# Kernel optimization log

Measured on AMD Instinct MI355X. Metric: run time of the kernel, lower is better.

Reference implementation:

```python
import jax, jax.numpy as jnp
import numpy as np
from jax import lax

T_D = 0.7          # condensation radius
T_B = 0.2          # min beta to seed a condensate
FEATURE_LENGTH = 9 # columns of raw features before the prediction block
N_FEAT = 17        # n_ccoords = N_FEAT - 14 = 3
N_EVENTS = 16
POINTS_PER_EVENT = 65536


def setup_inputs() -> dict:
    key = jax.random.key(0)
    N = N_EVENTS * POINTS_PER_EVENT
    # uniform [0,1): betas in [0,1), ccoords in the unit cube -> realistic clustering
    x = jax.random.uniform(key, (N, N_FEAT), dtype=jnp.float32)
    row_splits = (jnp.arange(N_EVENTS + 1) * POINTS_PER_EVENT).astype(jnp.int32)
    return {"x": x, "row_splits": row_splits}


def _build_condensates(ccoords, betas, radius, min_beta):
    """Greedy NMS-like condensation, vectorized over events.
    ccoords: [E, P, C] float; betas: [E, P] float.
    Returns asso [E,P] int32 (index of assigned condensate, -1 = noise) and
    iscond [E,P] bool (condensation point flags).
    """
    E, P, _ = ccoords.shape
    r2 = radius * radius

    def masked_beta(asso):
        return jnp.where(asso < 0, betas, -1.0)

    def cond_fn(state):
        asso, _ = state
        return jnp.any(jnp.max(masked_beta(asso), axis=1) >= min_beta)

    def body_fn(state):
        asso, iscond = state
        mb = masked_beta(asso)                     # [E,P]
        ref = jnp.argmax(mb, axis=1)               # [E] highest-beta unassigned point
        valid = jnp.take_along_axis(mb, ref[:, None], axis=1)[:, 0] >= min_beta  # [E]
        refc = jnp.take_along_axis(ccoords, ref[:, None, None], axis=1)          # [E,1,C]
        distsq = jnp.sum((ccoords - refc) ** 2, axis=-1)                          # [E,P]
        assign = (asso < 0) & (distsq <= r2) & valid[:, None]
        asso = jnp.where(assign, ref[:, None].astype(jnp.int32), asso)
        newcond = (jnp.arange(P)[None, :] == ref[:, None]) & valid[:, None]
        return asso, iscond | newcond

    asso0 = jnp.full((E, P), -1, dtype=jnp.int32)
    iscond0 = jnp.zeros((E, P), dtype=jnp.bool_)
    return lax.while_loop(cond_fn, body_fn, (asso0, iscond0))


def reference(x, row_splits):
    E = row_splits.shape[0] - 1
    N, F = x.shape
    P = N // E  # uniform events (RaggedConstructTensor equivalent for equal splits)
    n_ccoords = F - 14
    x_pred = x[:, FEATURE_LENGTH:]
    n_pred = x_pred.shape[-1]
    betas = x_pred[:, 0].reshape(E, P)
    ccoords = x_pred[:, n_pred - n_ccoords:].reshape(E, P, n_ccoords)

    asso, iscond = _build_condensates(ccoords, betas, T_D, T_B)

    ncond = jnp.sum(iscond, axis=1).astype(jnp.int32)  # condensates per event
    out_row_splits = jnp.concatenate(
        [jnp.zeros((1,), jnp.int32), jnp.cumsum(ncond).astype(jnp.int32)])
    # jit-safe equivalent of dout = x[iscond > 0]: zero-mask non-condensates
    mask = iscond.reshape(-1, 1).astype(x.dtype)
    dout = x * mask  # [N, F], rows of non-condensates are zero
    return dout, out_row_splits
```

## Files before the change

### kernel.cpp

```cpp
#include <hip/hip_runtime.h>

typedef unsigned long long u64;
typedef unsigned int u32;

static constexpr int NF = 17;
static constexpr int BCOL = 9;
static constexpr int CCOL = 14;
static constexpr int CONDCAP = 256;
static constexpr int REFCAP = 256;
static constexpr int CANDCAP = 6144;
static constexpr int RPB = 512;
static constexpr int FT = 1024;
static constexpr int KB = 8;
static constexpr int LCAP = 7168;

#define T_B_F  ((float)0.2)
#define R2_F   ((float)(0.7*0.7))
#define TAU0_F ((float)0.93)

__device__ __forceinline__ u64 kmax(u64 a, u64 b){ return a > b ? a : b; }

__device__ __forceinline__ u64 shfl_down_u64(u64 v, int off){
    u32 lo = (u32)v, hi = (u32)(v >> 32);
    lo = __shfl_down(lo, off, 64);
    hi = __shfl_down(hi, off, 64);
    return ((u64)hi << 32) | lo;
}

__device__ __forceinline__ u64 shfl_u64(u64 v, int lane){
    u32 lo = (u32)v, hi = (u32)(v >> 32);
    lo = __shfl(lo, lane, 64);
    hi = __shfl(hi, lane, 64);
    return ((u64)hi << 32) | lo;
}

__device__ __forceinline__ u64 waveReduceMax(u64 k){
    #pragma unroll
    for (int off = 32; off > 0; off >>= 1){
        u64 o = shfl_down_u64(k, off);
        if (o > k) k = o;
    }
    return k;
}

__device__ __forceinline__ void waveReduceMaxPair(u64 &k, int &p){
    #pragma unroll
    for (int off = 32; off > 0; off >>= 1){
        u64 ok = shfl_down_u64(k, off);
        int op = __shfl_down(p, off, 64);
        if (ok > k){ k = ok; p = op; }
    }
}

__device__ __forceinline__ float dist2(float cx, float cy, float cz,
                                       float rx, float ry, float rz){
    #pragma clang fp contract(off)
    float dx = cx - rx, dy = cy - ry, dz = cz - rz;
    float sx = dx * dx, sy = dy * dy, sz = dz * dz;
    return (sx + sy) + sz;
}

__device__ __forceinline__ u64 makeKey(float beta, u32 idx){
    return ((u64)__float_as_uint(beta) << 32) | (u64)(0xFFFFFFFFu - idx);
}

__global__ void k_init(u32* ws){
    int t = threadIdx.x;
    if (t < 1024) ws[t] = 0;
}

__global__ __launch_bounds__(512) void k_filter(
    const float4* __restrict__ x4, float4* __restrict__ out4,
    int* __restrict__ cnt0, float4* __restrict__ cA, int* __restrict__ iA,
    int* __restrict__ candCnt, int* __restrict__ candI,
    int P, int chunksPerEvent)
{
    __shared__ float lds[RPB * NF];
    __shared__ int swc[8], swb[8], sbase;
    __shared__ int swc2[8], swb2[8], sbase2;

    int e = blockIdx.x / chunksPerEvent;
    int chunk = blockIdx.x % chunksPerEvent;
    int rowStart = chunk * RPB;
    size_t tile4 = (size_t)blockIdx.x * (RPB * NF / 4);

    float4* lds4 = (float4*)lds;
    const int N4 = RPB * NF / 4;
    float4 z = make_float4(0.f, 0.f, 0.f, 0.f);
    for (int i = threadIdx.x; i < N4; i += 512){
        lds4[i] = x4[tile4 + i];
        out4[tile4 + i] = z;
    }
    __syncthreads();

    int tid = threadIdx.x, lid = tid & 63, wid = tid >> 6;
    float be = lds[tid*NF+BCOL];
    float cx = lds[tid*NF+CCOL], cy = lds[tid*NF+CCOL+1], cz = lds[tid*NF+CCOL+2];
    bool kp = (be >= T_B_F);
    bool cd = (be >= TAU0_F);
    u64 bal  = __ballot(kp);
    u64 bal2 = __ballot(cd);
    if (lid == 0){ swc[wid] = __popcll(bal); swc2[wid] = __popcll(bal2); }
    __syncthreads();
    if (tid == 0){
        int tot = 0, tot2 = 0;
        for (int w = 0; w < 8; w++){
            swb[w] = tot;  tot  += swc[w];
            swb2[w] = tot2; tot2 += swc2[w];
        }
        sbase  = tot  ? atomicAdd(&cnt0[e], tot)     : 0;
        sbase2 = tot2 ? atomicAdd(&candCnt[e], tot2) : 0;
    }
    __syncthreads();
    u64 lm = (1ull << lid) - 1;
    if (kp){
        int pos = sbase + swb[wid] + __popcll(bal & lm);
        size_t eoff = (size_t)e * P;
        cA[eoff + pos] = make_float4(cx, cy, cz, be);
        iA[eoff + pos] = rowStart + tid;
    }
    if (cd){
        int pos = sbase2 + swb2[wid] + __popcll(bal2 & lm);
        if (pos < CANDCAP) candI[e * CANDCAP + pos] = rowStart + tid;
    }
}

__global__ __launch_bounds__(1024) void k_resolve(
    const float* __restrict__ x, const int* __restrict__ candCnt,
    const int* __restrict__ candI, int* __restrict__ nrefs,
    int* __restrict__ condlist, float* __restrict__ refXg,
    float* __restrict__ refYg, float* __restrict__ refZg, int P)
{
    __shared__ u64 skey[CANDCAP];
    __shared__ float sx[CANDCAP], sy[CANDCAP], sz[CANDCAP];
    __shared__ u64 wk[16]; __shared__ int wp[16];
    __shared__ float rfx[REFCAP], rfy[REFCAP], rfz[REFCAP];
    __shared__ int rci[REFCAP];
    __shared__ int snr;

    int e = blockIdx.x;
    int tid = threadIdx.x, lid = tid & 63, wid = tid >> 6;
    int m = candCnt[e];
    if (m > CANDCAP || m == 0){ if (tid == 0) nrefs[e] = 0; return; }

    u64 bk = 0; int bp = 0;
    for (int i = tid; i < m; i += FT){
        int idx = candI[e * CANDCAP + i];
        size_t rb = ((size_t)e * P + idx) * NF;
        float be = x[rb + BCOL];
        u64 k = makeKey(be, (u32)idx);
        skey[i] = k;
        sx[i] = x[rb + CCOL]; sy[i] = x[rb + CCOL + 1]; sz[i] = x[rb + CCOL + 2];
        if (k > bk){ bk = k; bp = i; }
    }
    waveReduceMaxPair(bk, bp);
    if (lid == 0){ wk[wid] = bk; wp[wid] = bp; }
    __syncthreads();

    if (wid == 0){
        u64 key = (lid < 16) ? wk[lid] : 0;
        int mp  = (lid < 16) ? wp[lid] : 0;
        waveReduceMaxPair(key, mp);
        key = shfl_u64(key, 0); mp = __shfl(mp, 0, 64);

        int n = m, nr = 0;
        while (key){
            if (nr == REFCAP) break;
            float rx = sx[mp], ry = sy[mp], rz = sz[mp];
            if (lid == 0){
                rfx[nr] = rx; rfy[nr] = ry; rfz[nr] = rz;
                rci[nr] = (int)(0xFFFFFFFFu - (u32)key);
            }
            nr++;
            u64 nk = 0; int np = -1; int alive = 0;
            for (int i0 = 0; i0 < n; i0 += 64){
                int i = i0 + lid;
                bool inb = i < n;
                int ii = inb ? i : 0;
                u64 k2 = skey[ii];
                float xx = sx[ii], yy = sy[ii], zz = sz[ii];
                bool keep = inb && !(dist2(xx, yy, zz, rx, ry, rz) <= R2_F);
                u64 b = __ballot(keep);
                if (keep){
                    int pos = alive + __popcll(b & ((1ull << lid) - 1));
                    skey[pos] = k2; sx[pos] = xx; sy[pos] = yy; sz[pos] = zz;
                    if (k2 > nk){ nk = k2; np = pos; }
                }
                alive += __popcll(b);
            }
            waveReduceMaxPair(nk, np);
            key = shfl_u64(nk, 0); mp = __shfl(np, 0, 64);
            n = alive;
        }
        if (lid == 0) snr = nr;
    }
    __syncthreads();
    int nr = snr;
    for (int i = tid; i < nr; i += FT){
        refXg[e*REFCAP + i] = rfx[i];
        refYg[e*REFCAP + i] = rfy[i];
        refZg[e*REFCAP + i] = rfz[i];
        condlist[e*CONDCAP + i] = rci[i];
    }
    if (tid == 0) nrefs[e] = nr;
}

__global__ __launch_bounds__(256) void k_kill(
    const float4* __restrict__ cA, const int* __restrict__ iA,
    float4* __restrict__ cB, int* __restrict__ iB,
    const int* __restrict__ cnt0, int* __restrict__ cnt1,
    u64* __restrict__ argmax1, const int* __restrict__ nrefs,
    const float* __restrict__ refXg, const float* __restrict__ refYg,
    const float* __restrict__ refZg, int P, int bpe)
{
    __shared__ float rfx[REFCAP], rfy[REFCAP], rfz[REFCAP];
    __shared__ int swc[4], swb[4], sbase;
    __shared__ u64 sred[4];

    int e = blockIdx.x / bpe;
    int c = blockIdx.x % bpe;
    int n = cnt0[e];
    if (c * 256 >= n) return;
    int nr = nrefs[e];
    for (int i = threadIdx.x; i < nr; i += 256){
        rfx[i] = refXg[e*REFCAP + i];
        rfy[i] = refYg[e*REFCAP + i];
        rfz[i] = refZg[e*REFCAP + i];
    }
    __syncthreads();

    int tid = threadIdx.x, lid = tid & 63, wid = tid >> 6;
    size_t eoff = (size_t)e * P;
    int stride = bpe * 256;

    float4 cc[KB]; int ixv[KB]; bool kp[KB]; u64 bal[KB];
    int wcnt = 0; u64 lk = 0;
    #pragma unroll
    for (int k = 0; k < KB; k++){
        int i = c * 256 + tid + k * stride;
        bool inb = i < n;
        int ii = inb ? i : 0;
        cc[k] = cA[eoff + ii]; ixv[k] = iA[eoff + ii];
        bool alive = inb;
        for (int r = 0; r < nr; r++){
            if (alive && dist2(cc[k].x, cc[k].y, cc[k].z, rfx[r], rfy[r], rfz[r]) <= R2_F)
                alive = false;
        }
        kp[k] = alive;
        bal[k] = __ballot(alive);
        wcnt += __popcll(bal[k]);
        if (alive) lk = kmax(lk, makeKey(cc[k].w, (u32)ixv[k]));
    }
    u64 kw = waveReduceMax(lk);
    if (lid == 0){ swc[wid] = wcnt; sred[wid] = kw; }
    __syncthreads();
    if (tid == 0){
        int tot = 0;
        for (int w = 0; w < 4; w++){ swb[w] = tot; tot += swc[w]; }
        sbase = tot ? atomicAdd(&cnt1[e], tot) : 0;
        u64 mm = kmax(kmax(sred[0], sred[1]), kmax(sred[2], sred[3]));
        if (mm) atomicMax(&argmax1[e], mm);
    }
    __syncthreads();
    int pos = sbase + swb[wid];
    u64 lm = (1ull << lid) - 1;
    #pragma unroll
    for (int k = 0; k < KB; k++){
        if (kp[k]){
            int p_ = pos + __popcll(bal[k] & lm);
            cB[eoff + p_] = cc[k]; iB[eoff + p_] = ixv[k];
        }
        pos += __popcll(bal[k]);
    }
}

__global__ __launch_bounds__(1024) void k_finish2(
    const float* __restrict__ x,
    float4* cB, int* iB, float4* cA, int* iA,
    const u64* __restrict__ argmax1, const int* __restrict__ cnt1,
    const int* __restrict__ nrefs, int* __restrict__ ncond,
    const int* __restrict__ condlistG, int* __restrict__ done,
    float* __restrict__ out, int P, int E)
{
    __shared__ u64 skey[LCAP];
    __shared__ float sx[LCAP], sy[LCAP], sz[LCAP];
    __shared__ u64 sred[16];
    __shared__ int condL[CONDCAP];
    __shared__ int scnt, snc;
    __shared__ u64 skeyb;
    __shared__ float srefc[3];

    int e = blockIdx.x;
    int tid = threadIdx.x, lid = tid & 63, wid = tid >> 6;
    int n = cnt1[e];
    u64 key = argmax1[e];
    float4* cIn = cB + (size_t)e * P; int* iIn = iB + (size_t)e * P;
    float4* cOut = cA + (size_t)e * P; int* iOut = iA + (size_t)e * P;

    int nr0 = nrefs[e];
    for (int i = tid; i < nr0; i += FT) condL[i] = condlistG[e*CONDCAP + i];
    if (tid == 0) snc = nr0;
    __syncthreads();

    while (n > LCAP){
        float betaRef = __uint_as_float((u32)(key >> 32));
        if (!(betaRef >= T_B_F)) break;
        u32 refIdx = 0xFFFFFFFFu - (u32)(key & 0xFFFFFFFFu);
        if (tid == 0){
            if (snc < CONDCAP) condL[snc] = (int)refIdx;
            snc++;
            size_t rbase = ((size_t)e * P + refIdx) * NF;
            srefc[0] = x[rbase + CCOL];
            srefc[1] = x[rbase + CCOL + 1];
            srefc[2] = x[rbase + CCOL + 2];
            scnt = 0;
        }
        __syncthreads();
        float rx = srefc[0], ry = srefc[1], rz = srefc[2];
        u64 localKey = 0;
        for (int i = tid; i < n; i += FT){
            float4 cc = cIn[i]; int idx = iIn[i];
            float d2 = dist2(cc.x, cc.y, cc.z, rx, ry, rz);
            bool keep = !(d2 <= R2_F);
            u64 bal = __ballot(keep);
            int cw = __popcll(bal);
            int b_ = 0;
            if (lid == 0) b_ = cw ? atomicAdd(&scnt, cw) : 0;
            b_ = __shfl(b_, 0, 64);
            if (keep){
                int pos = b_ + __popcll(bal & ((1ull << lid) - 1));
                cOut[pos] = cc; iOut[pos] = idx;
                localKey = kmax(localKey, makeKey(cc.w, (u32)idx));
            }
        }
        u64 kw = waveReduceMax(localKey);
        if (lid == 0) sred[wid] = kw;
        __syncthreads();
        if (tid == 0){
            u64 m = 0;
            for (int i = 0; i < 16; i++) m = kmax(m, sred[i]);
            skeyb = m;
        }
        __syncthreads();
        key = skeyb; n = scnt;
        { float4* t = cIn; cIn = cOut; cOut = t; }
        { int* t = iIn; iIn = iOut; iOut = t; }
        __syncthreads();
    }

    float betaRef0 = __uint_as_float((u32)(key >> 32));
    if (betaRef0 >= T_B_F && n > 0){
        for (int i = tid; i < n; i += FT){
            float4 cc = cIn[i]; int idx = iIn[i];
            skey[i] = makeKey(cc.w, (u32)idx);
            sx[i] = cc.x; sy[i] = cc.y; sz[i] = cc.z;
        }
        __syncthreads();

        if (wid == 0){
            int snc_l = snc;
            int mp = -1;
            while (true){
                float betaRef = __uint_as_float((u32)(key >> 32));
                if (!(betaRef >= T_B_F)) break;
                u32 refIdx = 0xFFFFFFFFu - (u32)(key & 0xFFFFFFFFu);
                if (lid == 0 && snc_l < CONDCAP) condL[snc_l] = (int)refIdx;
                snc_l++;
                float rx, ry, rz;
                if (mp >= 0){ rx = sx[mp]; ry = sy[mp]; rz = sz[mp]; }
                else {
                    size_t rbase = ((size_t)e * P + refIdx) * NF;
                    rx = x[rbase + CCOL]; ry = x[rbase + CCOL + 1]; rz = x[rbase + CCOL + 2];
                }
                u64 bk = 0; int bp = -1;
                int alive = 0;
                for (int i0 = 0; i0 < n; i0 += 64){
                    int i = i0 + lid;
                    bool inb = i < n;
                    int ii = inb ? i : 0;
                    u64 k = skey[ii];
                    float xx = sx[ii], yy = sy[ii], zz = sz[ii];
                    float d2 = dist2(xx, yy, zz, rx, ry, rz);
                    bool keep = inb && !(d2 <= R2_F);
                    u64 b = __ballot(keep);
                    if (keep){
                        int pos = alive + __popcll(b & ((1ull << lid) - 1));
                        skey[pos] = k; sx[pos] = xx; sy[pos] = yy; sz[pos] = zz;
                        if (k > bk){ bk = k; bp = pos; }
                    }
                    alive += __popcll(b);
                }
                waveReduceMaxPair(bk, bp);
                key = shfl_u64(bk, 0);
                mp = __shfl(bp, 0, 64);
                n = alive;
            }
            if (lid == 0) snc = snc_l;
        }
    }
    __syncthreads();

    int ncT = snc;
    int ncc = ncT > CONDCAP ? CONDCAP : ncT;
    for (int i = tid; i < ncc * NF; i += FT){
        int j = i / NF, f = i - j * NF;
        int row = condL[j];
        size_t base = ((size_t)e * P + row) * NF;
        out[base + f] = x[base + f];
    }
    if (tid == 0){
        ncond[e] = ncT;
        __threadfence();
        int r = atomicAdd(done, 1);
        if (r == E - 1){
            size_t ob = (size_t)E * P * NF;
            int s = 0;
            out[ob] = 0.0f;
            for (int i = 0; i < E; i++){
                s += atomicAdd((int*)&ncond[i], 0);
                out[ob + i + 1] = (float)s;
            }
        }
    }
}

extern "C" void kernel_launch(void* const* d_in, const int* in_sizes, int n_in,
                              void* d_out, int out_size, void* d_ws, size_t ws_size,
                              hipStream_t stream) {
    const float* x = (const float*)d_in[0];
    int N = in_sizes[0] / NF;
    int E = in_sizes[1] - 1;
    int P = N / E;
    float* out = (float*)d_out;
    char* ws = (char*)d_ws;

    u64* argmax1 = (u64*)ws;
    int* cnt0    = (int*)(ws + 1024);
    int* cnt1    = (int*)(ws + 1280);
    int* candCnt = (int*)(ws + 1536);
    int* nrefs   = (int*)(ws + 1792);
    int* ncond   = (int*)(ws + 2048);
    int* done    = (int*)(ws + 2304);
    int* condlist= (int*)(ws + 4096);
    float* refXg = (float*)(ws + 20480);
    float* refYg = (float*)(ws + 36864);
    float* refZg = (float*)(ws + 53248);
    size_t listOff = 69632;
    size_t listElems = (size_t)E * P;
    float4* cA = (float4*)(ws + listOff);
    float4* cB = (float4*)(ws + listOff + listElems * 16);
    int* iA = (int*)(ws + listOff + listElems * 32);
    int* iB = (int*)(ws + listOff + listElems * 36);
    int* candI = iB;

    k_init<<<1, 1024, 0, stream>>>((u32*)ws);

    int chunksPerEvent = P / RPB;
    k_filter<<<E * chunksPerEvent, 512, 0, stream>>>(
        (const float4*)x, (float4*)out, cnt0, cA, iA, candCnt, candI, P, chunksPerEvent);

    k_resolve<<<E, 1024, 0, stream>>>(
        x, candCnt, candI, nrefs, condlist, refXg, refYg, refZg, P);

    int bpe = 32;
    k_kill<<<E * bpe, 256, 0, stream>>>(
        cA, iA, cB, iB, cnt0, cnt1, argmax1, nrefs, refXg, refYg, refZg, P, bpe);

    k_finish2<<<E, 1024, 0, stream>>>(
        x, cB, iB, cA, iA, argmax1, cnt1, nrefs, ncond, condlist, done, out, P, E);
}
```

Baseline: 196.6 us.

## Fuse kill and finish kernels via last-block-per-event, compact candidate coordinates

Merges the kill and finish kernels into one launch. In the merged kernel, the last block to finish for each event (tracked with a per-event atomic counter) runs the greedy tail with 256 threads and a smaller shared-memory cap. Candidate coordinates and betas are stored compactly in k_filter, so k_resolve no longer gathers them from x with strided reads. Zeroing the output is moved after the filter work and uses nontemporal stores. The kill phase now uses 64 blocks per event with 4 items per thread. The risk is that the serial tail runs with fewer threads and a smaller list cap (1536 versus 7168), which can mean more passes over global memory.

After: 253.0 us. 28.7% more time.

```diff
diff --git a/kernel.cpp b/kernel.cpp
--- a/kernel.cpp
+++ b/kernel.cpp
@@ -2,6 +2,7 @@
 
 typedef unsigned long long u64;
 typedef unsigned int u32;
+typedef float nfloat4 __attribute__((ext_vector_type(4)));
 
 static constexpr int NF = 17;
 static constexpr int BCOL = 9;
@@ -11,8 +12,10 @@
 static constexpr int CANDCAP = 6144;
 static constexpr int RPB = 512;
 static constexpr int FT = 1024;
-static constexpr int KB = 8;
-static constexpr int LCAP = 7168;
+static constexpr int TT = 256;
+static constexpr int BPE = 64;
+static constexpr int KB2 = 4;
+static constexpr int FCAP = 1536;
 
 #define T_B_F  ((float)0.2)
 #define R2_F   ((float)(0.7*0.7))
@@ -72,7 +75,7 @@
 __global__ __launch_bounds__(512) void k_filter(
     const float4* __restrict__ x4, float4* __restrict__ out4,
     int* __restrict__ cnt0, float4* __restrict__ cA, int* __restrict__ iA,
-    int* __restrict__ candCnt, int* __restrict__ candI,
+    int* __restrict__ candCnt, float4* __restrict__ candC, int* __restrict__ candI,
     int P, int chunksPerEvent)
 {
     __shared__ float lds[RPB * NF];
@@ -86,11 +89,8 @@
 
     float4* lds4 = (float4*)lds;
     const int N4 = RPB * NF / 4;
-    float4 z = make_float4(0.f, 0.f, 0.f, 0.f);
-    for (int i = threadIdx.x; i < N4; i += 512){
+    for (int i = threadIdx.x; i < N4; i += 512)
         lds4[i] = x4[tile4 + i];
-        out4[tile4 + i] = z;
-    }
     __syncthreads();
 
     int tid = threadIdx.x, lid = tid & 63, wid = tid >> 6;
@@ -121,15 +121,21 @@
     }
     if (cd){
         int pos = sbase2 + swb2[wid] + __popcll(bal2 & lm);
-        if (pos < CANDCAP) candI[e * CANDCAP + pos] = rowStart + tid;
-    }
+        if (pos < CANDCAP){
+            candC[(size_t)e * CANDCAP + pos] = make_float4(cx, cy, cz, be);
+            candI[(size_t)e * CANDCAP + pos] = rowStart + tid;
+        }
+    }
+    nfloat4 z = (nfloat4)0.f;
+    for (int i = tid; i < N4; i += 512)
+        __builtin_nontemporal_store(z, (nfloat4*)&out4[tile4 + i]);
 }
 
 __global__ __launch_bounds__(1024) void k_resolve(
-    const float* __restrict__ x, const int* __restrict__ candCnt,
-    const int* __restrict__ candI, int* __restrict__ nrefs,
+    const float4* __restrict__ candC, const int* __restrict__ candI,
+    const int* __restrict__ candCnt, int* __restrict__ nrefs,
     int* __restrict__ condlist, float* __restrict__ refXg,
-    float* __restrict__ refYg, float* __restrict__ refZg, int P)
+    float* __restrict__ refYg, float* __restrict__ refZg)
 {
     __shared__ u64 skey[CANDCAP];
     __shared__ float sx[CANDCAP], sy[CANDCAP], sz[CANDCAP];
@@ -145,12 +151,10 @@
 
     u64 bk = 0; int bp = 0;
     for (int i = tid; i < m; i += FT){
-        int idx = candI[e * CANDCAP + i];
-        size_t rb = ((size_t)e * P + idx) * NF;
-        float be = x[rb + BCOL];
-        u64 k = makeKey(be, (u32)idx);
+        float4 c = candC[(size_t)e * CANDCAP + i];
+        u64 k = makeKey(c.w, (u32)candI[(size_t)e * CANDCAP + i]);
         skey[i] = k;
-        sx[i] = x[rb + CCOL]; sy[i] = x[rb + CCOL + 1]; sz[i] = x[rb + CCOL + 2];
+        sx[i] = c.x; sy[i] = c.y; sz[i] = c.z;
         if (k > bk){ bk = k; bp = i; }
     }
     waveReduceMaxPair(bk, bp);
@@ -205,187 +209,171 @@
     if (tid == 0) nrefs[e] = nr;
 }
 
-__global__ __launch_bounds__(256) void k_kill(
-    const float4* __restrict__ cA, const int* __restrict__ iA,
-    float4* __restrict__ cB, int* __restrict__ iB,
+__global__ __launch_bounds__(256) void k_killfin(
+    const float* __restrict__ x,
+    float4* cA, int* iA, float4* cB, int* iB,
     const int* __restrict__ cnt0, int* __restrict__ cnt1,
     u64* __restrict__ argmax1, const int* __restrict__ nrefs,
     const float* __restrict__ refXg, const float* __restrict__ refYg,
-    const float* __restrict__ refZg, int P, int bpe)
+    const float* __restrict__ refZg,
+    int* __restrict__ ncond, const int* __restrict__ condlistG,
+    int* __restrict__ doneE, int* __restrict__ done,
+    float* __restrict__ out, int P, int E)
 {
     __shared__ float rfx[REFCAP], rfy[REFCAP], rfz[REFCAP];
     __shared__ int swc[4], swb[4], sbase;
     __shared__ u64 sred[4];
-
-    int e = blockIdx.x / bpe;
-    int c = blockIdx.x % bpe;
-    int n = cnt0[e];
-    if (c * 256 >= n) return;
-    int nr = nrefs[e];
-    for (int i = threadIdx.x; i < nr; i += 256){
-        rfx[i] = refXg[e*REFCAP + i];
-        rfy[i] = refYg[e*REFCAP + i];
-        rfz[i] = refZg[e*REFCAP + i];
-    }
-    __syncthreads();
-
-    int tid = threadIdx.x, lid = tid & 63, wid = tid >> 6;
-    size_t eoff = (size_t)e * P;
-    int stride = bpe * 256;
-
-    float4 cc[KB]; int ixv[KB]; bool kp[KB]; u64 bal[KB];
-    int wcnt = 0; u64 lk = 0;
-    #pragma unroll
-    for (int k = 0; k < KB; k++){
-        int i = c * 256 + tid + k * stride;
-        bool inb = i < n;
-        int ii = inb ? i : 0;
-        cc[k] = cA[eoff + ii]; ixv[k] = iA[eoff + ii];
-        bool alive = inb;
-        for (int r = 0; r < nr; r++){
-            if (alive && dist2(cc[k].x, cc[k].y, cc[k].z, rfx[r], rfy[r], rfz[r]) <= R2_F)
-                alive = false;
-        }
-        kp[k] = alive;
-        bal[k] = __ballot(alive);
-        wcnt += __popcll(bal[k]);
-        if (alive) lk = kmax(lk, makeKey(cc[k].w, (u32)ixv[k]));
-    }
-    u64 kw = waveReduceMax(lk);
-    if (lid == 0){ swc[wid] = wcnt; sred[wid] = kw; }
-    __syncthreads();
-    if (tid == 0){
-        int tot = 0;
-        for (int w = 0; w < 4; w++){ swb[w] = tot; tot += swc[w]; }
-        sbase = tot ? atomicAdd(&cnt1[e], tot) : 0;
-        u64 mm = kmax(kmax(sred[0], sred[1]), kmax(sred[2], sred[3]));
-        if (mm) atomicMax(&argmax1[e], mm);
-    }
-    __syncthreads();
-    int pos = sbase + swb[wid];
-    u64 lm = (1ull << lid) - 1;
-    #pragma unroll
-    for (int k = 0; k < KB; k++){
-        if (kp[k]){
-            int p_ = pos + __popcll(bal[k] & lm);
-            cB[eoff + p_] = cc[k]; iB[eoff + p_] = ixv[k];
-        }
-        pos += __popcll(bal[k]);
-    }
-}
-
-__global__ __launch_bounds__(1024) void k_finish2(
-    const float* __restrict__ x,
-    float4* cB, int* iB, float4* cA, int* iA,
-    const u64* __restrict__ argmax1, const int* __restrict__ cnt1,
-    const int* __restrict__ nrefs, int* __restrict__ ncond,
-    const int* __restrict__ condlistG, int* __restrict__ done,
-    float* __restrict__ out, int P, int E)
-{
-    __shared__ u64 skey[LCAP];
-    __shared__ float sx[LCAP], sy[LCAP], sz[LCAP];
-    __shared__ u64 sred[16];
+    __shared__ u64 fkey[FCAP];
+    __shared__ float fx[FCAP], fy[FCAP], fz[FCAP];
     __shared__ int condL[CONDCAP];
-    __shared__ int scnt, snc;
+    __shared__ int scnt, snc, slast;
     __shared__ u64 skeyb;
     __shared__ float srefc[3];
 
-    int e = blockIdx.x;
+    int e = blockIdx.x / BPE;
+    int c = blockIdx.x % BPE;
     int tid = threadIdx.x, lid = tid & 63, wid = tid >> 6;
-    int n = cnt1[e];
-    u64 key = argmax1[e];
-    float4* cIn = cB + (size_t)e * P; int* iIn = iB + (size_t)e * P;
-    float4* cOut = cA + (size_t)e * P; int* iOut = iA + (size_t)e * P;
-
-    int nr0 = nrefs[e];
-    for (int i = tid; i < nr0; i += FT) condL[i] = condlistG[e*CONDCAP + i];
-    if (tid == 0) snc = nr0;
-    __syncthreads();
-
-    while (n > LCAP){
+    int n = cnt0[e];
+    int nr = nrefs[e];
+    size_t eoff = (size_t)e * P;
+
+    if (c * TT < n){
+        for (int i = tid; i < nr; i += TT){
+            rfx[i] = refXg[e*REFCAP + i];
+            rfy[i] = refYg[e*REFCAP + i];
+            rfz[i] = refZg[e*REFCAP + i];
+        }
+        __syncthreads();
+        int stride = BPE * TT;
+        float4 cc[KB2]; int ixv[KB2]; bool kp[KB2]; u64 bal[KB2];
+        int wcnt = 0; u64 lk = 0;
+        #pragma unroll
+        for (int k = 0; k < KB2; k++){
+            int i = c * TT + tid + k * stride;
+            bool inb = i < n;
+            int ii = inb ? i : 0;
+            cc[k] = cA[eoff + ii]; ixv[k] = iA[eoff + ii];
+            bool alive = inb;
+            for (int r = 0; r < nr; r++)
+                if (alive && dist2(cc[k].x, cc[k].y, cc[k].z, rfx[r], rfy[r], rfz[r]) <= R2_F)
+                    alive = false;
+            kp[k] = alive;
+            bal[k] = __ballot(alive);
+            wcnt += __popcll(bal[k]);
+            if (alive) lk = kmax(lk, makeKey(cc[k].w, (u32)ixv[k]));
+        }
+        u64 kw = waveReduceMax(lk);
+        if (lid == 0){ swc[wid] = wcnt; sred[wid] = kw; }
+        __syncthreads();
+        if (tid == 0){
+            int tot = 0;
+            for (int w = 0; w < 4; w++){ swb[w] = tot; tot += swc[w]; }
+            sbase = tot ? atomicAdd(&cnt1[e], tot) : 0;
+            u64 mm = kmax(kmax(sred[0], sred[1]), kmax(sred[2], sred[3]));
+            if (mm) atomicMax(&argmax1[e], mm);
+        }
+        __syncthreads();
+        int pos = sbase + swb[wid];
+        u64 lm = (1ull << lid) - 1;
+        #pragma unroll
+        for (int k = 0; k < KB2; k++){
+            if (kp[k]){
+                int p_ = pos + __popcll(bal[k] & lm);
+                cB[eoff + p_] = cc[k]; iB[eoff + p_] = ixv[k];
+            }
+            pos += __popcll(bal[k]);
+        }
+    }
+    __threadfence();
+    if (tid == 0) slast = (atomicAdd(&doneE[e], 1) == BPE - 1) ? 1 : 0;
+    __syncthreads();
+    if (!slast) return;
+    __threadfence();
+
+    int n1 = atomicAdd(&cnt1[e], 0);
+    u64 key = atomicMax(&argmax1[e], 0ull);
+    for (int i = tid; i < nr; i += TT) condL[i] = condlistG[e*CONDCAP + i];
+    if (tid == 0) snc = nr;
+    __syncthreads();
+
+    float4* cIn = cB + eoff; int* iIn = iB + eoff;
+    float4* cOut = cA + eoff; int* iOut = iA + eoff;
+
+    while (n1 > FCAP){
         float betaRef = __uint_as_float((u32)(key >> 32));
         if (!(betaRef >= T_B_F)) break;
-        u32 refIdx = 0xFFFFFFFFu - (u32)(key & 0xFFFFFFFFu);
+        u32 refIdx = 0xFFFFFFFFu - (u32)key;
         if (tid == 0){
             if (snc < CONDCAP) condL[snc] = (int)refIdx;
             snc++;
-            size_t rbase = ((size_t)e * P + refIdx) * NF;
-            srefc[0] = x[rbase + CCOL];
-            srefc[1] = x[rbase + CCOL + 1];
-            srefc[2] = x[rbase + CCOL + 2];
+            size_t rb = (eoff + refIdx) * NF;
+            srefc[0] = x[rb + CCOL]; srefc[1] = x[rb + CCOL + 1]; srefc[2] = x[rb + CCOL + 2];
             scnt = 0;
         }
         __syncthreads();
         float rx = srefc[0], ry = srefc[1], rz = srefc[2];
         u64 localKey = 0;
-        for (int i = tid; i < n; i += FT){
+        for (int i = tid; i < n1; i += TT){
             float4 cc = cIn[i]; int idx = iIn[i];
-            float d2 = dist2(cc.x, cc.y, cc.z, rx, ry, rz);
-            bool keep = !(d2 <= R2_F);
-            u64 bal = __ballot(keep);
-            int cw = __popcll(bal);
+            bool keep = !(dist2(cc.x, cc.y, cc.z, rx, ry, rz) <= R2_F);
+            u64 b = __ballot(keep);
+            int cw = __popcll(b);
             int b_ = 0;
             if (lid == 0) b_ = cw ? atomicAdd(&scnt, cw) : 0;
             b_ = __shfl(b_, 0, 64);
             if (keep){
-                int pos = b_ + __popcll(bal & ((1ull << lid) - 1));
+                int pos = b_ + __popcll(b & ((1ull << lid) - 1));
                 cOut[pos] = cc; iOut[pos] = idx;
                 localKey = kmax(localKey, makeKey(cc.w, (u32)idx));
             }
         }
-        u64 kw = waveReduceMax(localKey);
-        if (lid == 0) sred[wid] = kw;
-        __syncthreads();
-        if (tid == 0){
-            u64 m = 0;
-            for (int i = 0; i < 16; i++) m = kmax(m, sred[i]);
-            skeyb = m;
-        }
-        __syncthreads();
-        key = skeyb; n = scnt;
+        u64 kw2 = waveReduceMax(localKey);
+        if (lid == 0) sred[wid] = kw2;
+        __syncthreads();
+        if (tid == 0) skeyb = kmax(kmax(sred[0], sred[1]), kmax(sred[2], sred[3]));
+        __syncthreads();
+        key = skeyb; n1 = scnt;
         { float4* t = cIn; cIn = cOut; cOut = t; }
         { int* t = iIn; iIn = iOut; iOut = t; }
         __syncthreads();
     }
 
-    float betaRef0 = __uint_as_float((u32)(key >> 32));
-    if (betaRef0 >= T_B_F && n > 0){
-        for (int i = tid; i < n; i += FT){
+    float b0 = __uint_as_float((u32)(key >> 32));
+    if (b0 >= T_B_F && n1 > 0){
+        for (int i = tid; i < n1; i += TT){
             float4 cc = cIn[i]; int idx = iIn[i];
-            skey[i] = makeKey(cc.w, (u32)idx);
-            sx[i] = cc.x; sy[i] = cc.y; sz[i] = cc.z;
-        }
-        __syncthreads();
-
+            fkey[i] = makeKey(cc.w, (u32)idx);
+            fx[i] = cc.x; fy[i] = cc.y; fz[i] = cc.z;
+        }
+        __syncthreads();
         if (wid == 0){
             int snc_l = snc;
             int mp = -1;
+            int nn = n1;
             while (true){
                 float betaRef = __uint_as_float((u32)(key >> 32));
                 if (!(betaRef >= T_B_F)) break;
-                u32 refIdx = 0xFFFFFFFFu - (u32)(key & 0xFFFFFFFFu);
+                u32 refIdx = 0xFFFFFFFFu - (u32)key;
                 if (lid == 0 && snc_l < CONDCAP) condL[snc_l] = (int)refIdx;
                 snc_l++;
                 float rx, ry, rz;
-                if (mp >= 0){ rx = sx[mp]; ry = sy[mp]; rz = sz[mp]; }
+                if (mp >= 0){ rx = fx[mp]; ry = fy[mp]; rz = fz[mp]; }
                 else {
-                    size_t rbase = ((size_t)e * P + refIdx) * NF;
-                    rx = x[rbase + CCOL]; ry = x[rbase + CCOL + 1]; rz = x[rbase + CCOL + 2];
+                    size_t rb = (eoff + refIdx) * NF;
+                    rx = x[rb + CCOL]; ry = x[rb + CCOL + 1]; rz = x[rb + CCOL + 2];
                 }
-                u64 bk = 0; int bp = -1;
-                int alive = 0;
-                for (int i0 = 0; i0 < n; i0 += 64){
+                u64 bk = 0; int bp = -1; int alive = 0;
+                for (int i0 = 0; i0 < nn; i0 += 64){
                     int i = i0 + lid;
-                    bool inb = i < n;
+                    bool inb = i < nn;
                     int ii = inb ? i : 0;
-                    u64 k = skey[ii];
-                    float xx = sx[ii], yy = sy[ii], zz = sz[ii];
-                    float d2 = dist2(xx, yy, zz, rx, ry, rz);
-                    bool keep = inb && !(d2 <= R2_F);
+                    u64 k = fkey[ii];
+                    float xx = fx[ii], yy = fy[ii], zz = fz[ii];
+                    bool keep = inb && !(dist2(xx, yy, zz, rx, ry, rz) <= R2_F);
                     u64 b = __ballot(keep);
                     if (keep){
                         int pos = alive + __popcll(b & ((1ull << lid) - 1));
-                        skey[pos] = k; sx[pos] = xx; sy[pos] = yy; sz[pos] = zz;
+                        fkey[pos] = k; fx[pos] = xx; fy[pos] = yy; fz[pos] = zz;
                         if (k > bk){ bk = k; bp = pos; }
                     }
                     alive += __popcll(b);
@@ -393,7 +381,7 @@
                 waveReduceMaxPair(bk, bp);
                 key = shfl_u64(bk, 0);
                 mp = __shfl(bp, 0, 64);
-                n = alive;
+                nn = alive;
             }
             if (lid == 0) snc = snc_l;
         }
@@ -402,10 +390,10 @@
 
     int ncT = snc;
     int ncc = ncT > CONDCAP ? CONDCAP : ncT;
-    for (int i = tid; i < ncc * NF; i += FT){
+    for (int i = tid; i < ncc * NF; i += TT){
         int j = i / NF, f = i - j * NF;
         int row = condL[j];
-        size_t base = ((size_t)e * P + row) * NF;
+        size_t base = (eoff + row) * NF;
         out[base + f] = x[base + f];
     }
     if (tid == 0){
@@ -417,7 +405,7 @@
             int s = 0;
             out[ob] = 0.0f;
             for (int i = 0; i < E; i++){
-                s += atomicAdd((int*)&ncond[i], 0);
+                s += atomicAdd(&ncond[i], 0);
                 out[ob + i + 1] = (float)s;
             }
         }
@@ -440,32 +428,32 @@
     int* candCnt = (int*)(ws + 1536);
     int* nrefs   = (int*)(ws + 1792);
     int* ncond   = (int*)(ws + 2048);
-    int* done    = (int*)(ws + 2304);
+    int* doneE   = (int*)(ws + 2304);
+    int* done    = (int*)(ws + 2560);
     int* condlist= (int*)(ws + 4096);
     float* refXg = (float*)(ws + 20480);
     float* refYg = (float*)(ws + 36864);
     float* refZg = (float*)(ws + 53248);
-    size_t listOff = 69632;
+    float4* candC = (float4*)(ws + 69632);
+    int* candI    = (int*)(ws + 69632 + (size_t)16 * CANDCAP * 16);
+    size_t listOff = 4194304;
     size_t listElems = (size_t)E * P;
     float4* cA = (float4*)(ws + listOff);
     float4* cB = (float4*)(ws + listOff + listElems * 16);
     int* iA = (int*)(ws + listOff + listElems * 32);
     int* iB = (int*)(ws + listOff + listElems * 36);
-    int* candI = iB;
 
     k_init<<<1, 1024, 0, stream>>>((u32*)ws);
 
     int chunksPerEvent = P / RPB;
     k_filter<<<E * chunksPerEvent, 512, 0, stream>>>(
-        (const float4*)x, (float4*)out, cnt0, cA, iA, candCnt, candI, P, chunksPerEvent);
+        (const float4*)x, (float4*)out, cnt0, cA, iA, candCnt, candC, candI,
+        P, chunksPerEvent);
 
     k_resolve<<<E, 1024, 0, stream>>>(
-        x, candCnt, candI, nrefs, condlist, refXg, refYg, refZg, P);
-
-    int bpe = 32;
-    k_kill<<<E * bpe, 256, 0, stream>>>(
-        cA, iA, cB, iB, cnt0, cnt1, argmax1, nrefs, refXg, refYg, refZg, P, bpe);
-
-    k_finish2<<<E, 1024, 0, stream>>>(
-        x, cB, iB, cA, iA, argmax1, cnt1, nrefs, ncond, condlist, done, out, P, E);
-}
+        candC, candI, candCnt, nrefs, condlist, refXg, refYg, refZg);
+
+    k_killfin<<<E * BPE, 256, 0, stream>>>(
+        x, cA, iA, cB, iB, cnt0, cnt1, argmax1, nrefs, refXg, refYg, refZg,
+        ncond, condlist, doneE, done, out, P, E);
+}
```
